# Optimization experiments

Measured on AMD Instinct MI355X. Metric: run time of the kernel, lower is better.

## Reference

```python
import jax, jax.numpy as jnp
import numpy as np

N, E, C, A, F = 10000, 128000, 128, 10, 8
LDIMS = (1, 3, 5)  # 0e, 1o, 2e spherical-harmonic block sizes
NPATH = len(LDIMS)


def setup_inputs() -> dict:
    key = jax.random.key(0)
    ks = jax.random.split(key, 16)
    rn = lambda k, s, sc=1.0: jax.random.normal(k, s, dtype=jnp.float32) * sc
    inp = {
        "node_attrs": rn(ks[0], (N, A)),
        "node_feats": rn(ks[1], (N, C)),
        "edge_attrs_real": rn(ks[2], (E, 9)),
        "edge_attrs_imag": rn(ks[3], (E, 9)),
        "edge_feats": jax.random.uniform(ks[4], (E, F), dtype=jnp.float32),
        "edge_index": jax.random.randint(ks[5], (2, E), 0, N, dtype=jnp.int32),
        # learned parameters (e3nn 1/sqrt(fan_in) normalization folded into init)
        "W_up": rn(ks[6], (C, C), 1.0 / np.sqrt(C)),            # o3.Linear on 128x0e
        "W_skip": rn(ks[7], (C, A, C), 1.0 / np.sqrt(C * A)),    # FullyConnectedTensorProduct
        "W_mlp1": rn(ks[8], (F, 64), 1.0 / np.sqrt(F)),
        "W_mlp2": rn(ks[9], (64, 64), 1.0 / 8.0),
        "W_mlp3": rn(ks[10], (64, 64), 1.0 / 8.0),
        "W_mlp4": rn(ks[11], (64, NPATH * C), 1.0 / 8.0),        # -> conv_tp.weight_numel = 384
        "W_lin0": rn(ks[12], (C, C), 1.0 / np.sqrt(C)),          # o3.Linear per-l blocks
        "W_lin1": rn(ks[13], (C, C), 1.0 / np.sqrt(C)),
        "W_lin2": rn(ks[14], (C, C), 1.0 / np.sqrt(C)),
    }
    return inp


def _conv_tp(x, y, w):
    """scalar(128x0e) x sh(0e+1o+2e) uvu tensor product with per-edge weights.
    x: [E,C] sender scalars, y: [E,9] edge sh, w: [E,NPATH,C] -> [E, C*9] irreps_mid layout."""
    outs, off = [], 0
    for l, d in enumerate(LDIMS):
        yl = y[:, off:off + d]                      # [E,d]
        off += d
        xw = x * w[:, l]                            # [E,C]
        outs.append((xw[:, :, None] * yl[:, None, :]).reshape(-1, C * d))
    return jnp.concatenate(outs, axis=-1)           # [E, C*(1+3+5)]


def _linear_irreps(m, Ws):
    """o3.Linear mixing channels within each l block. m: [N, C*9] -> [N, C, 9]."""
    outs, off = [], 0
    for l, d in enumerate(LDIMS):
        blk = m[:, off:off + C * d].reshape(-1, C, d)  # [N,C,d]
        off += C * d
        outs.append(jnp.einsum('num,uk->nkm', blk, Ws[l]))
    return jnp.concatenate(outs, axis=-1)              # [N,C,9] (reshape_irreps layout)


def reference(node_attrs, node_feats, edge_attrs_real, edge_attrs_imag, edge_feats,
              edge_index, W_up, W_skip, W_mlp1, W_mlp2, W_mlp3, W_mlp4,
              W_lin0, W_lin1, W_lin2):
    sender, receiver = edge_index[0], edge_index[1]
    # skip connection: FullyConnectedTensorProduct(node_feats 128x0e, node_attrs 10x0e)
    sc = jnp.einsum('nu,nv,uvk->nk', node_feats, node_attrs, W_skip)
    # linear_up
    h = node_feats @ W_up
    # per-edge tensor-product weights from radial MLP (silu hidden layers, linear out)
    t = jax.nn.silu(edge_feats @ W_mlp1)
    t = jax.nn.silu(t @ W_mlp2)
    t = jax.nn.silu(t @ W_mlp3)
    tpw = (t @ W_mlp4).reshape(-1, NPATH, C)
    # gather senders, tensor product for real and imag edge attrs
    xs = h[sender]
    mji_r = _conv_tp(xs, edge_attrs_real, tpw)
    mji_i = _conv_tp(xs, edge_attrs_imag, tpw)
    # scatter-sum to receivers
    msg_r = jax.ops.segment_sum(mji_r, receiver, num_segments=N)
    msg_i = jax.ops.segment_sum(mji_i, receiver, num_segments=N)
    # output linear + reshape_irreps -> [N, C, 9]
    Ws = (W_lin0, W_lin1, W_lin2)
    out_r = _linear_irreps(msg_r, Ws)
    out_i = _linear_irreps(msg_i, Ws)
    return out_r, out_i, sc
```

## Files before the change

kernel.cpp:

```cpp
#include <hip/hip_runtime.h>
#include <hip/hip_bf16.h>

#define N_NODES 10000
#define N_EDGES 128000
#define C_DIM   128

typedef __attribute__((ext_vector_type(8))) short bf16x8;
typedef __attribute__((ext_vector_type(4))) float f32x4;


__device__ __forceinline__ float silu_f(float x) {
  return x / (1.f + __expf(-x));
}

__device__ __forceinline__ unsigned short f2bf(float x) {
  __hip_bfloat16 b = __float2bfloat16(x);
  return *(unsigned short*)&b;
}

__device__ __forceinline__ bf16x8 pack8(float4 lo, float4 hi) {
  bf16x8 r;
  r[0] = (short)f2bf(lo.x); r[1] = (short)f2bf(lo.y);
  r[2] = (short)f2bf(lo.z); r[3] = (short)f2bf(lo.w);
  r[4] = (short)f2bf(hi.x); r[5] = (short)f2bf(hi.y);
  r[6] = (short)f2bf(hi.z); r[7] = (short)f2bf(hi.w);
  return r;
}

__global__ __launch_bounds__(256) void k_h(const float* __restrict__ feats,
                                           const float* __restrict__ Wup,
                                           float* __restrict__ h) {
  __shared__ float sF[32][129];
  int tid = threadIdx.x;
  int n0 = blockIdx.x * 32;
  int nmax = N_NODES - n0; if (nmax > 32) nmax = 32;
  for (int i = tid; i < 32 * 128; i += 256) {
    int nn = i >> 7, kk = i & 127;
    sF[nn][kk] = (nn < nmax) ? feats[(n0 + nn) * 128 + kk] : 0.f;
  }
  __syncthreads();
  int n = tid >> 3;
  int jb = (tid & 7) * 16;
  if (n < nmax) {
    float4 acc[4] = {};
    for (int k = 0; k < 128; k++) {
      float a = sF[n][k];
      #pragma unroll
      for (int jg = 0; jg < 4; jg++) {
        float4 w = *(const float4*)&Wup[k * 128 + jb + jg * 4];
        acc[jg].x += a * w.x; acc[jg].y += a * w.y;
        acc[jg].z += a * w.z; acc[jg].w += a * w.w;
      }
    }
    #pragma unroll
    for (int jg = 0; jg < 4; jg++)
      *(float4*)&h[(n0 + n) * 128 + jb + jg * 4] = acc[jg];
  }
}

__global__ void k_wcvt(const float* __restrict__ Wskip,
                       const float* __restrict__ Wl0,
                       const float* __restrict__ Wl1,
                       const float* __restrict__ Wl2,
                       unsigned short* __restrict__ wbT,
                       unsigned short* __restrict__ wlT) {
  int idx = blockIdx.x * 256 + threadIdx.x;
  if (idx < 163840) {
    int j = idx >> 7, k = idx & 127;
    int u = j / 10, v = j - u * 10;
    wbT[k * 1280 + v * 128 + u] = f2bf(Wskip[idx]);
  } else if (idx < 163840 + 49152) {
    int t = idx - 163840;
    int l = t >> 14, r = t & 16383;
    int u = r >> 7, k = r & 127;
    const float* W = (l == 0) ? Wl0 : (l == 1) ? Wl1 : Wl2;
    wlT[(l * 128 + k) * 128 + u] = f2bf(W[r]);
  }
}

__global__ void k_wcvt2(const float* __restrict__ W1, const float* __restrict__ W2,
                        const float* __restrict__ W3, const float* __restrict__ W4,
                        unsigned short* __restrict__ w1f, unsigned short* __restrict__ w2f,
                        unsigned short* __restrict__ w3f, unsigned short* __restrict__ w4f) {
  int idx = blockIdx.x * 256 + threadIdx.x;
  if (idx < 2048) {
    int ct = idx >> 9, r = idx & 511, n = r >> 5, t = r & 31;
    w1f[idx] = (t < 8) ? f2bf(W1[t * 64 + ct * 16 + n]) : (unsigned short)0;
  } else if (idx < 6144) {
    int j = idx - 2048;
    int ctks = j >> 9, r = j & 511, n = r >> 5, t = r & 31;
    int ct = ctks >> 1, ks = ctks & 1;
    w2f[j] = f2bf(W2[(ks * 32 + t) * 64 + ct * 16 + n]);
  } else if (idx < 10240) {
    int j = idx - 6144;
    int ctks = j >> 9, r = j & 511, n = r >> 5, t = r & 31;
    int ct = ctks >> 1, ks = ctks & 1;
    w3f[j] = f2bf(W3[(ks * 32 + t) * 64 + ct * 16 + n]);
  } else if (idx < 34816) {
    int j = idx - 10240;
    int ctks = j >> 9, r = j & 511, n = r >> 5, t = r & 31;
    int ct = ctks >> 1, ks = ctks & 1;
    w4f[j] = f2bf(W4[(ks * 32 + t) * 384 + ct * 16 + n]);
  }
}

__global__ __launch_bounds__(256) void k_sc(const float* __restrict__ f,
                                            const float* __restrict__ at,
                                            const unsigned short* __restrict__ wbT,
                                            float* __restrict__ sc_out) {
  int tid = threadIdx.x;
  int w = tid >> 6, lane = tid & 63;
  int l15 = lane & 15, quad = lane >> 4;
  int n0 = blockIdx.x * 32;

  int nrow[2];
  #pragma unroll
  for (int t = 0; t < 2; t++) {
    int n = n0 + 16 * t + l15;
    nrow[t] = (n < N_NODES) ? n : (N_NODES - 1);
  }
  float4 fA[2][4][2];
  #pragma unroll
  for (int t = 0; t < 2; t++)
    #pragma unroll
    for (int ks = 0; ks < 4; ks++) {
      fA[t][ks][0] = *(const float4*)&f[nrow[t] * 128 + ks * 32 + quad * 8];
      fA[t][ks][1] = *(const float4*)&f[nrow[t] * 128 + ks * 32 + quad * 8 + 4];
    }

  f32x4 acc[2][2] = {};
  #pragma unroll 1
  for (int c = 0; c < 10; c++) {
    float av[2];
    #pragma unroll
    for (int t = 0; t < 2; t++) av[t] = at[nrow[t] * 10 + c];
    bf16x8 af[2][4];
    #pragma unroll
    for (int t = 0; t < 2; t++)
      #pragma unroll
      for (int ks = 0; ks < 4; ks++) {
        float4 lo = fA[t][ks][0], hi = fA[t][ks][1];
        lo.x *= av[t]; lo.y *= av[t]; lo.z *= av[t]; lo.w *= av[t];
        hi.x *= av[t]; hi.y *= av[t]; hi.z *= av[t]; hi.w *= av[t];
        af[t][ks] = pack8(lo, hi);
      }
    #pragma unroll
    for (int kt = 0; kt < 2; kt++) {
      int kcol = w * 32 + kt * 16 + l15;
      #pragma unroll
      for (int ks = 0; ks < 4; ks++) {
        bf16x8 bf = *(const bf16x8*)&wbT[kcol * 1280 + c * 128 + ks * 32 + quad * 8];
        #pragma unroll
        for (int t = 0; t < 2; t++)
          acc[t][kt] = __builtin_amdgcn_mfma_f32_16x16x32_bf16(af[t][ks], bf,
                                                               acc[t][kt], 0, 0, 0);
      }
    }
  }
  #pragma unroll
  for (int t = 0; t < 2; t++)
    #pragma unroll
    for (int kt = 0; kt < 2; kt++) {
      int kcol = w * 32 + kt * 16 + l15;
      #pragma unroll
      for (int reg = 0; reg < 4; reg++) {
        int n = n0 + 16 * t + quad * 4 + reg;
        if (n < N_NODES) sc_out[n * 128 + kcol] = acc[t][kt][reg];
      }
    }
}

__global__ __launch_bounds__(256) void k_mlp(const float* __restrict__ ef,
                                             const unsigned short* __restrict__ w1f,
                                             const unsigned short* __restrict__ w2f,
                                             const unsigned short* __restrict__ w3f,
                                             const unsigned short* __restrict__ w4f,
                                             unsigned short* __restrict__ tpw) {
  __shared__ unsigned short sA[128][72];
  __shared__ unsigned short sB[128][72];
  int tid = threadIdx.x;
  int w = tid >> 6, lane = tid & 63;
  int l15 = lane & 15, quad = lane >> 4;
  int e0 = blockIdx.x * 128;
  int fragoff = l15 * 32 + quad * 8;
  int rb = w * 32;

  {
    bf16x8 af[2];
    #pragma unroll
    for (int rt = 0; rt < 2; rt++) {
      bf16x8 a = {};
      if (quad == 0) {
        int e = e0 + rb + rt * 16 + l15;
        float4 lo = *(const float4*)&ef[e * 8];
        float4 hi = *(const float4*)&ef[e * 8 + 4];
        a = pack8(lo, hi);
      }
      af[rt] = a;
    }
    f32x4 ac[2][4] = {};
    #pragma unroll
    for (int ct = 0; ct < 4; ct++) {
      bf16x8 b = *(const bf16x8*)&w1f[ct * 512 + fragoff];
      ac[0][ct] = __builtin_amdgcn_mfma_f32_16x16x32_bf16(af[0], b, ac[0][ct], 0, 0, 0);
      ac[1][ct] = __builtin_amdgcn_mfma_f32_16x16x32_bf16(af[1], b, ac[1][ct], 0, 0, 0);
    }
    #pragma unroll
    for (int rt = 0; rt < 2; rt++)
      #pragma unroll
      for (int ct = 0; ct < 4; ct++)
        #pragma unroll
        for (int reg = 0; reg < 4; reg++)
          sA[rb + rt * 16 + quad * 4 + reg][ct * 16 + l15] =
              f2bf(silu_f(ac[rt][ct][reg]));
  }
  __syncthreads();

  #pragma unroll 1
  for (int layer = 0; layer < 2; layer++) {
    unsigned short (*src)[72] = (layer == 0) ? sA : sB;
    unsigned short (*dst)[72] = (layer == 0) ? sB : sA;
    const unsigned short* wf = (layer == 0) ? w2f : w3f;
    bf16x8 a2[2][2];
    #pragma unroll
    for (int rt = 0; rt < 2; rt++)
      #pragma unroll
      for (int ks = 0; ks < 2; ks++)
        a2[rt][ks] = *(const bf16x8*)&src[rb + rt * 16 + l15][ks * 32 + quad * 8];
    f32x4 ac[2][4] = {};
    #pragma unroll
    for (int ct = 0; ct < 4; ct++)
      #pragma unroll
      for (int ks = 0; ks < 2; ks++) {
        bf16x8 b = *(const bf16x8*)&wf[(ct * 2 + ks) * 512 + fragoff];
        ac[0][ct] = __builtin_amdgcn_mfma_f32_16x16x32_bf16(a2[0][ks], b, ac[0][ct], 0, 0, 0);
        ac[1][ct] = __builtin_amdgcn_mfma_f32_16x16x32_bf16(a2[1][ks], b, ac[1][ct], 0, 0, 0);
      }
    #pragma unroll
    for (int rt = 0; rt < 2; rt++)
      #pragma unroll
      for (int ct = 0; ct < 4; ct++)
        #pragma unroll
        for (int reg = 0; reg < 4; reg++)
          dst[rb + rt * 16 + quad * 4 + reg][ct * 16 + l15] =
              f2bf(silu_f(ac[rt][ct][reg]));
    __syncthreads();
  }

  bf16x8 a4[2][2];
  #pragma unroll
  for (int rt = 0; rt < 2; rt++)
    #pragma unroll
    for (int ks = 0; ks < 2; ks++)
      a4[rt][ks] = *(const bf16x8*)&sA[rb + rt * 16 + l15][ks * 32 + quad * 8];

  #pragma unroll 1
  for (int ch = 0; ch < 6; ch++) {
    f32x4 ac[2][4] = {};
    #pragma unroll
    for (int ct = 0; ct < 4; ct++)
      #pragma unroll
      for (int ks = 0; ks < 2; ks++) {
        bf16x8 b = *(const bf16x8*)&w4f[((ch * 4 + ct) * 2 + ks) * 512 + fragoff];
        ac[0][ct] = __builtin_amdgcn_mfma_f32_16x16x32_bf16(a4[0][ks], b, ac[0][ct], 0, 0, 0);
        ac[1][ct] = __builtin_amdgcn_mfma_f32_16x16x32_bf16(a4[1][ks], b, ac[1][ct], 0, 0, 0);
      }
    #pragma unroll
    for (int rt = 0; rt < 2; rt++)
      #pragma unroll
      for (int ct = 0; ct < 4; ct++)
        #pragma unroll
        for (int reg = 0; reg < 4; reg++)
          sB[rb + rt * 16 + quad * 4 + reg][ct * 16 + l15] = f2bf(ac[rt][ct][reg]);
    __syncthreads();
    #pragma unroll
    for (int v = 0; v < 4; v++) {
      int idx = v * 256 + tid;
      int e = idx >> 3, cg = idx & 7;
      uint4 p = *(const uint4*)&sB[e][cg * 8];
      *(uint4*)&tpw[(size_t)(e0 + e) * 384 + ch * 64 + cg * 8] = p;
    }
    __syncthreads();
  }
}

__global__ void k_hist(const int* __restrict__ recv, int* __restrict__ counts) {
  int e = blockIdx.x * 256 + threadIdx.x;
  if (e < N_EDGES) atomicAdd(&counts[recv[e]], 1);
}

__global__ __launch_bounds__(1024) void k_scan(const int* __restrict__ counts,
                                               int* __restrict__ offsets,
                                               int* __restrict__ cursor) {
  __shared__ int part[1024];
  int tid = threadIdx.x;
  int base = tid * 10;
  int local[10]; int s = 0;
  #pragma unroll
  for (int i = 0; i < 10; i++) {
    int idx = base + i;
    int c = (idx < N_NODES) ? counts[idx] : 0;
    local[i] = s; s += c;
  }
  part[tid] = s;
  __syncthreads();
  for (int off = 1; off < 1024; off <<= 1) {
    int v = (tid >= off) ? part[tid - off] : 0;
    __syncthreads();
    part[tid] += v;
    __syncthreads();
  }
  int pre = (tid > 0) ? part[tid - 1] : 0;
  #pragma unroll
  for (int i = 0; i < 10; i++) {
    int idx = base + i;
    if (idx < N_NODES) { int o = pre + local[i]; offsets[idx] = o; cursor[idx] = o; }
  }
  if (tid == 1023) offsets[N_NODES] = part[1023];
}

__global__ void k_scatter(const int* __restrict__ recv, int* __restrict__ cursor,
                          int* __restrict__ order) {
  int e = blockIdx.x * 256 + threadIdx.x;
  if (e < N_EDGES) {
    int idx = atomicAdd(&cursor[recv[e]], 1);
    order[idx] = e;
  }
}

__device__ __forceinline__ void edge_acc(int e, int u,
    const float* __restrict__ h, const unsigned short* __restrict__ tpw,
    const float* __restrict__ yr, const float* __restrict__ yi,
    const int* __restrict__ send, float* mr, float* mi) {
  int s = send[e];
  float xv = h[s * 128 + u];
  __hip_bfloat16 b0 = *(const __hip_bfloat16*)&tpw[e * 384 + u];
  __hip_bfloat16 b1 = *(const __hip_bfloat16*)&tpw[e * 384 + 128 + u];
  __hip_bfloat16 b2 = *(const __hip_bfloat16*)&tpw[e * 384 + 256 + u];
  float xw0 = xv * __bfloat162float(b0);
  float xw1 = xv * __bfloat162float(b1);
  float xw2 = xv * __bfloat162float(b2);
  const float* yre = &yr[e * 9];
  const float* yie = &yi[e * 9];
  mr[0] += xw0 * yre[0]; mi[0] += xw0 * yie[0];
  #pragma unroll
  for (int m = 1; m < 4; m++) { mr[m] += xw1 * yre[m]; mi[m] += xw1 * yie[m]; }
  #pragma unroll
  for (int m = 4; m < 9; m++) { mr[m] += xw2 * yre[m]; mi[m] += xw2 * yie[m]; }
}

__global__ __launch_bounds__(128) void k_gather(
    const float* __restrict__ h, const unsigned short* __restrict__ tpw,
    const float* __restrict__ yr, const float* __restrict__ yi,
    const int* __restrict__ send, const int* __restrict__ offsets,
    const int* __restrict__ order,
    unsigned short* __restrict__ msg) {
  int u = threadIdx.x;
  int n = blockIdx.x;
  float mr[9] = {}, mi[9] = {};
  int e0 = offsets[n], e1 = offsets[n + 1];
  int jj = e0;
  for (; jj + 1 < e1; jj += 2) {
    int ea = order[jj];
    int eb = order[jj + 1];
    edge_acc(ea, u, h, tpw, yr, yi, send, mr, mi);
    edge_acc(eb, u, h, tpw, yr, yi, send, mr, mi);
  }
  if (jj < e1) {
    int ea = order[jj];
    edge_acc(ea, u, h, tpw, yr, yi, send, mr, mi);
  }
  int g = n >> 3, i = n & 7;
  unsigned short* mg = msg + (size_t)g * 144 * 128;
  mg[(i * 2 + 0) * 128 + u] = f2bf(mr[0]);
  mg[(i * 2 + 1) * 128 + u] = f2bf(mi[0]);
  #pragma unroll
  for (int m = 1; m < 4; m++) {
    mg[(16 + i * 6 + (m - 1)) * 128 + u] = f2bf(mr[m]);
    mg[(16 + i * 6 + 3 + (m - 1)) * 128 + u] = f2bf(mi[m]);
  }
  #pragma unroll
  for (int m = 4; m < 9; m++) {
    mg[(64 + i * 10 + (m - 4)) * 128 + u] = f2bf(mr[m]);
    mg[(64 + i * 10 + 5 + (m - 4)) * 128 + u] = f2bf(mi[m]);
  }
}

#define LIN_ROWPAD 1156
__global__ __launch_bounds__(256) void k_lin(const unsigned short* __restrict__ msg,
                                             const unsigned short* __restrict__ wlT,
                                             float* __restrict__ out) {
  __shared__ float so[2 * 8 * LIN_ROWPAD];
  int tid = threadIdx.x;
  int w = tid >> 6, lane = tid & 63;
  int l15 = lane & 15, quad = lane >> 4;
  int g = blockIdx.x;

  bf16x8 bfr[3][2][4];
  #pragma unroll
  for (int l = 0; l < 3; l++)
    #pragma unroll
    for (int kt = 0; kt < 2; kt++)
      #pragma unroll
      for (int ks = 0; ks < 4; ks++) {
        int ncol = w * 32 + kt * 16 + l15;
        bfr[l][kt][ks] = *(const bf16x8*)&wlT[(l * 128 + ncol) * 128 + ks * 32 + quad * 8];
      }

  const unsigned short* mg = msg + (size_t)g * 144 * 128;

  #pragma unroll
  for (int tile = 0; tile < 9; tile++) {
    const int l = (tile == 0) ? 0 : (tile < 4) ? 1 : 2;
    const int rbase = tile * 16;
    bf16x8 af[4];
    #pragma unroll
    for (int ks = 0; ks < 4; ks++)
      af[ks] = *(const bf16x8*)&mg[(rbase + l15) * 128 + ks * 32 + quad * 8];
    f32x4 acc0 = {}, acc1 = {};
    #pragma unroll
    for (int ks = 0; ks < 4; ks++) {
      acc0 = __builtin_amdgcn_mfma_f32_16x16x32_bf16(af[ks], bfr[l][0][ks], acc0, 0, 0, 0);
      acc1 = __builtin_amdgcn_mfma_f32_16x16x32_bf16(af[ks], bfr[l][1][ks], acc1, 0, 0, 0);
    }
    #pragma unroll
    for (int reg = 0; reg < 4; reg++) {
      int r = rbase + quad * 4 + reg;
      int c, ni, m;
      if (tile == 0) { ni = (r & 15) >> 1; c = r & 1; m = 0; }
      else if (tile < 4) {
        int q = r - 16; ni = q / 6; int rem = q - ni * 6;
        c = rem >= 3; m = 1 + rem - (c ? 3 : 0);
      } else {
        int q = r - 64; ni = q / 10; int rem = q - ni * 10;
        c = rem >= 5; m = 4 + rem - (c ? 5 : 0);
      }
      int k0 = w * 32 + l15;
      float* ob = &so[(c * 8 + ni) * LIN_ROWPAD + m];
      ob[(k0)      * 9] = acc0[reg];
      ob[(k0 + 16) * 9] = acc1[reg];
    }
  }
  __syncthreads();
  #pragma unroll
  for (int v = 0; v < 18; v++) {
    int idx = v * 256 + tid;
    int c = idx / 2304;
    int rem = idx - c * 2304;
    int ni = rem / 288;
    int off4 = rem - ni * 288;
    float4 p = *(const float4*)&so[(c * 8 + ni) * LIN_ROWPAD + off4 * 4];
    *(float4*)&out[(size_t)c * 11520000 + ((size_t)g * 8 + ni) * 1152 + (size_t)off4 * 4] = p;
  }
}

extern "C" void kernel_launch(void* const* d_in, const int* in_sizes, int n_in,
                              void* d_out, int out_size, void* d_ws, size_t ws_size,
                              hipStream_t stream) {
  const float* node_attrs = (const float*)d_in[0];
  const float* node_feats = (const float*)d_in[1];
  const float* ear   = (const float*)d_in[2];
  const float* eai   = (const float*)d_in[3];
  const float* ef    = (const float*)d_in[4];
  const int*   eidx  = (const int*)d_in[5];
  const float* Wup   = (const float*)d_in[6];
  const float* Wskip = (const float*)d_in[7];
  const float* W1    = (const float*)d_in[8];
  const float* W2    = (const float*)d_in[9];
  const float* W3    = (const float*)d_in[10];
  const float* W4    = (const float*)d_in[11];
  const float* Wl0   = (const float*)d_in[12];
  const float* Wl1   = (const float*)d_in[13];
  const float* Wl2   = (const float*)d_in[14];
  float* out = (float*)d_out;

  char* ws = (char*)d_ws;
  float*          h       = (float*)ws;
  unsigned short* tpw     = (unsigned short*)(ws + 5120000);
  unsigned short* msg     = (unsigned short*)(ws + 103424000);
  unsigned short* wlT     = (unsigned short*)(ws + 149504000);
  unsigned short* wbT     = (unsigned short*)(ws + 149602304);
  int*            counts  = (int*)(ws + 149929984);
  int*            offsets = (int*)(ws + 149969984);
  int*            cursor  = (int*)(ws + 150010112);
  int*            order   = (int*)(ws + 150050112);
  unsigned short* w1f     = (unsigned short*)(ws + 150562816);
  unsigned short* w2f     = (unsigned short*)(ws + 150566912);
  unsigned short* w3f     = (unsigned short*)(ws + 150575104);
  unsigned short* w4f     = (unsigned short*)(ws + 150583296);

  const int* send = eidx;
  const int* recv = eidx + N_EDGES;

  hipMemsetAsync(counts, 0, N_NODES * sizeof(int), stream);
  k_hist<<<dim3(500), dim3(256), 0, stream>>>(recv, counts);
  k_scan<<<dim3(1), dim3(1024), 0, stream>>>(counts, offsets, cursor);
  k_scatter<<<dim3(500), dim3(256), 0, stream>>>(recv, cursor, order);
  k_wcvt<<<dim3(832), dim3(256), 0, stream>>>(Wskip, Wl0, Wl1, Wl2, wbT, wlT);
  k_wcvt2<<<dim3(136), dim3(256), 0, stream>>>(W1, W2, W3, W4, w1f, w2f, w3f, w4f);
  k_h<<<dim3(313), dim3(256), 0, stream>>>(node_feats, Wup, h);
  k_sc<<<dim3(313), dim3(256), 0, stream>>>(node_feats, node_attrs, wbT,
                                            out + 2 * 11520000);
  k_mlp<<<dim3(1000), dim3(256), 0, stream>>>(ef, w1f, w2f, w3f, w4f, tpw);
  k_gather<<<dim3(10000), dim3(128), 0, stream>>>(h, tpw, ear, eai, send, offsets,
                                                  order, msg);
  k_lin<<<dim3(1250), dim3(256), 0, stream>>>(msg, wlT, out);
  (void)in_sizes; (void)n_in; (void)out_size; (void)ws_size;
}
```

Baseline: 395.0 us.

## Permute edge data into receiver-sorted order so gather reads are contiguous

Adds a kernel that reorders sender indices and real/imag edge attributes into receiver-sorted order, packed as 20-float rows. The radial MLP now reads edge features through the sort order, so its per-edge weights come out already sorted. The gather kernel then streams tpw, y and sender indices contiguously instead of chasing the indirection. In exchange there is an extra permutation pass, random reads of edge features in the MLP, and reuse of the output buffer as scratch before it is overwritten.

```diff
diff --git a/kernel.cpp b/kernel.cpp
--- a/kernel.cpp
+++ b/kernel.cpp
@@ -16,6 +16,11 @@
 __device__ __forceinline__ unsigned short f2bf(float x) {
   __hip_bfloat16 b = __float2bfloat16(x);
   return *(unsigned short*)&b;
+}
+
+__device__ __forceinline__ float bf2f(unsigned short u) {
+  __hip_bfloat16 b = *(__hip_bfloat16*)&u;
+  return __bfloat162float(b);
 }
 
 __device__ __forceinline__ bf16x8 pack8(float4 lo, float4 hi) {
@@ -171,6 +176,7 @@
 }
 
 __global__ __launch_bounds__(256) void k_mlp(const float* __restrict__ ef,
+                                             const int* __restrict__ order,
                                              const unsigned short* __restrict__ w1f,
                                              const unsigned short* __restrict__ w2f,
                                              const unsigned short* __restrict__ w3f,
@@ -191,7 +197,8 @@
     for (int rt = 0; rt < 2; rt++) {
       bf16x8 a = {};
       if (quad == 0) {
-        int e = e0 + rb + rt * 16 + l15;
+        int pos = e0 + rb + rt * 16 + l15;
+        int e = order[pos];
         float4 lo = *(const float4*)&ef[e * 8];
         float4 hi = *(const float4*)&ef[e * 8 + 4];
         a = pack8(lo, hi);
@@ -328,32 +335,63 @@
   }
 }
 
-__device__ __forceinline__ void edge_acc(int e, int u,
+__global__ __launch_bounds__(256) void k_yg(const float* __restrict__ yr,
+                                            const float* __restrict__ yi,
+                                            const int* __restrict__ send,
+                                            const int* __restrict__ order,
+                                            float* __restrict__ y2,
+                                            int* __restrict__ ss) {
+  __shared__ float sy[256][20];
+  int tid = threadIdx.x;
+  int p0 = blockIdx.x * 256;
+  int e = order[p0 + tid];
+  ss[p0 + tid] = send[e];
+  #pragma unroll
+  for (int m = 0; m < 9; m++) {
+    sy[tid][m] = yr[e * 9 + m];
+    sy[tid][9 + m] = yi[e * 9 + m];
+  }
+  sy[tid][18] = 0.f; sy[tid][19] = 0.f;
+  __syncthreads();
+  #pragma unroll
+  for (int v = 0; v < 5; v++) {
+    int idx = v * 256 + tid;
+    int r = idx / 5, c2 = idx - r * 5;
+    float4 p4 = *(const float4*)&sy[r][c2 * 4];
+    *(float4*)&y2[(size_t)(p0 + r) * 20 + c2 * 4] = p4;
+  }
+}
+
+__device__ __forceinline__ void edge_acc(int pos, int u,
     const float* __restrict__ h, const unsigned short* __restrict__ tpw,
-    const float* __restrict__ yr, const float* __restrict__ yi,
-    const int* __restrict__ send, float* mr, float* mi) {
-  int s = send[e];
+    const float* __restrict__ y2, const int* __restrict__ ss,
+    float* mr, float* mi) {
+  int s = ss[pos];
+  const float* yy = &y2[(size_t)pos * 20];
+  float4 v0 = *(const float4*)&yy[0];
+  float4 v1 = *(const float4*)&yy[4];
+  float4 v2 = *(const float4*)&yy[8];
+  float4 v3 = *(const float4*)&yy[12];
+  float4 v4 = *(const float4*)&yy[16];
+  float t0 = bf2f(tpw[(size_t)pos * 384 + u]);
+  float t1 = bf2f(tpw[(size_t)pos * 384 + 128 + u]);
+  float t2 = bf2f(tpw[(size_t)pos * 384 + 256 + u]);
   float xv = h[s * 128 + u];
-  __hip_bfloat16 b0 = *(const __hip_bfloat16*)&tpw[e * 384 + u];
-  __hip_bfloat16 b1 = *(const __hip_bfloat16*)&tpw[e * 384 + 128 + u];
-  __hip_bfloat16 b2 = *(const __hip_bfloat16*)&tpw[e * 384 + 256 + u];
-  float xw0 = xv * __bfloat162float(b0);
-  float xw1 = xv * __bfloat162float(b1);
-  float xw2 = xv * __bfloat162float(b2);
-  const float* yre = &yr[e * 9];
-  const float* yie = &yi[e * 9];
-  mr[0] += xw0 * yre[0]; mi[0] += xw0 * yie[0];
-  #pragma unroll
-  for (int m = 1; m < 4; m++) { mr[m] += xw1 * yre[m]; mi[m] += xw1 * yie[m]; }
-  #pragma unroll
-  for (int m = 4; m < 9; m++) { mr[m] += xw2 * yre[m]; mi[m] += xw2 * yie[m]; }
-}
-
-__global__ __launch_bounds__(128) void k_gather(
+  float xw0 = xv * t0, xw1 = xv * t1, xw2 = xv * t2;
+  mr[0] += xw0 * v0.x;
+  mr[1] += xw1 * v0.y; mr[2] += xw1 * v0.z; mr[3] += xw1 * v0.w;
+  mr[4] += xw2 * v1.x; mr[5] += xw2 * v1.y; mr[6] += xw2 * v1.z;
+  mr[7] += xw2 * v1.w; mr[8] += xw2 * v2.x;
+  mi[0] += xw0 * v2.y;
+  mi[1] += xw1 * v2.z; mi[2] += xw1 * v2.w; mi[3] += xw1 * v3.x;
+  mi[4] += xw2 * v3.y; mi[5] += xw2 * v3.z; mi[6] += xw2 * v3.w;
+  mi[7] += xw2 * v4.x; mi[8] += xw2 * v4.y;
+}
+
+__global__ __launch_bounds__(128, 4) void k_gather(
     const float* __restrict__ h, const unsigned short* __restrict__ tpw,
-    const float* __restrict__ yr, const float* __restrict__ yi,
-    const int* __restrict__ send, const int* __restrict__ offsets,
-    const int* __restrict__ order,
+    const float* __restrict__ y2, const int* __restrict__ ss,
+    const int* __restrict__ offsets,
     unsigned short* __restrict__ msg) {
   int u = threadIdx.x;
   int n = blockIdx.x;
@@ -361,14 +399,11 @@
   int e0 = offsets[n], e1 = offsets[n + 1];
   int jj = e0;
   for (; jj + 1 < e1; jj += 2) {
-    int ea = order[jj];
-    int eb = order[jj + 1];
-    edge_acc(ea, u, h, tpw, yr, yi, send, mr, mi);
-    edge_acc(eb, u, h, tpw, yr, yi, send, mr, mi);
+    edge_acc(jj, u, h, tpw, y2, ss, mr, mi);
+    edge_acc(jj + 1, u, h, tpw, y2, ss, mr, mi);
   }
   if (jj < e1) {
-    int ea = order[jj];
-    edge_acc(ea, u, h, tpw, yr, yi, send, mr, mi);
+    edge_acc(jj, u, h, tpw, y2, ss, mr, mi);
   }
   int g = n >> 3, i = n & 7;
   unsigned short* mg = msg + (size_t)g * 144 * 128;
@@ -489,6 +524,9 @@
   unsigned short* w3f     = (unsigned short*)(ws + 150575104);
   unsigned short* w4f     = (unsigned short*)(ws + 150583296);
 
+  float* y2 = (float*)d_out;
+  int*   ss = (int*)((char*)d_out + 10240000);
+
   const int* send = eidx;
   const int* recv = eidx + N_EDGES;
 
@@ -496,14 +534,14 @@
   k_hist<<<dim3(500), dim3(256), 0, stream>>>(recv, counts);
   k_scan<<<dim3(1), dim3(1024), 0, stream>>>(counts, offsets, cursor);
   k_scatter<<<dim3(500), dim3(256), 0, stream>>>(recv, cursor, order);
+  k_yg<<<dim3(500), dim3(256), 0, stream>>>(ear, eai, send, order, y2, ss);
   k_wcvt<<<dim3(832), dim3(256), 0, stream>>>(Wskip, Wl0, Wl1, Wl2, wbT, wlT);
   k_wcvt2<<<dim3(136), dim3(256), 0, stream>>>(W1, W2, W3, W4, w1f, w2f, w3f, w4f);
   k_h<<<dim3(313), dim3(256), 0, stream>>>(node_feats, Wup, h);
   k_sc<<<dim3(313), dim3(256), 0, stream>>>(node_feats, node_attrs, wbT,
                                             out + 2 * 11520000);
-  k_mlp<<<dim3(1000), dim3(256), 0, stream>>>(ef, w1f, w2f, w3f, w4f, tpw);
-  k_gather<<<dim3(10000), dim3(128), 0, stream>>>(h, tpw, ear, eai, send, offsets,
-                                                  order, msg);
+  k_mlp<<<dim3(1000), dim3(256), 0, stream>>>(ef, order, w1f, w2f, w3f, w4f, tpw);
+  k_gather<<<dim3(10000), dim3(128), 0, stream>>>(h, tpw, y2, ss, offsets, msg);
   k_lin<<<dim3(1250), dim3(256), 0, stream>>>(msg, wlT, out);
   (void)in_sizes; (void)n_in; (void)out_size; (void)ws_size;
 }
```

Result: faster. 367.7 us (-6.9%).
